# Optimization experiments

Measured on AMD Instinct MI355X. Metric: run time of the kernel, lower is better.

The kernel has to match this reference:

```python
import jax, jax.numpy as jnp
import numpy as np

B, S, H, F, E, K = 4, 2048, 512, 2048, 8, 2


def setup_inputs() -> dict:
    key = jax.random.key(0)
    ks = jax.random.split(key, 6)
    s_h = 1.0 / np.sqrt(H)
    s_f = 1.0 / np.sqrt(F)
    return {
        "x": jax.random.normal(ks[0], (B, S, H), dtype=jnp.float32),
        "router_w": jax.random.uniform(ks[1], (E, H), jnp.float32, -s_h, s_h),
        "fc1_w": jax.random.uniform(ks[2], (E, F, H), jnp.float32, -s_h, s_h),
        "fc1_b": jax.random.uniform(ks[3], (E, F), jnp.float32, -s_h, s_h),
        "fc2_w": jax.random.uniform(ks[4], (E, H, F), jnp.float32, -s_f, s_f),
        "fc2_b": jax.random.uniform(ks[5], (E, H), jnp.float32, -s_f, s_f),
    }


def reference(x, router_w, fc1_w, fc1_b, fc2_w, fc2_b):
    # Router: Linear (no bias), softmax over experts, top-k, renormalize.
    logits = jnp.einsum("bsh,eh->bse", x, router_w)           # [B,S,E]
    probs = jax.nn.softmax(logits, axis=-1)                    # [B,S,E]
    topk_p, topk_i = jax.lax.top_k(probs, K)                   # [B,S,K]
    topk_p = topk_p / (jnp.sum(topk_p, axis=-1, keepdims=True) + 1e-9)

    # Original loop runs every expert FFN on all tokens and masks;
    # mathematically identical: dense per-expert FFN, then gather+combine.
    h1 = jnp.einsum("bsh,efh->bsef", x, fc1_w) + fc1_b         # [B,S,E,F]
    a = jax.nn.gelu(h1, approximate=False)                     # exact erf GELU (torch nn.GELU default)
    y = jnp.einsum("bsef,ehf->bseh", a, fc2_w) + fc2_b         # [B,S,E,H]

    sel = jnp.take_along_axis(y, topk_i[..., None], axis=2)    # [B,S,K,H]
    output = jnp.sum(topk_p[..., None] * sel, axis=2)          # [B,S,H]
    return output, probs, topk_i
```

## Files before the change

### kernel.cpp

```cpp
#include <hip/hip_runtime.h>

#define T_TOKENS 8192
#define HD 512
#define FD 2048
#define NE 8
#define CAP 8192
#define CSTRIDE 32

#define BM 128

typedef __attribute__((ext_vector_type(8))) short short8;
typedef __attribute__((ext_vector_type(4))) float f32x4;

__device__ __forceinline__ ushort f2bf(float f) {
  union { float f; unsigned u; } v; v.f = f;
  unsigned u = v.u;
  return (ushort)((u + 0x7fffu + ((u >> 16) & 1u)) >> 16);
}

__device__ __forceinline__ unsigned pack_trunc(float lo, float hi) {
  union { float f; unsigned u; } a, b; a.f = lo; b.f = hi;
  return __builtin_amdgcn_perm(b.u, a.u, 0x07060302);
}

__global__ void cvt_bf16(const float4* __restrict__ src, ushort4* __restrict__ dst, int n4) {
  int i = blockIdx.x * blockDim.x + threadIdx.x;
  int st = gridDim.x * blockDim.x;
  for (; i < n4; i += st) {
    float4 v = src[i];
    ushort4 o;
    o.x = f2bf(v.x); o.y = f2bf(v.y); o.z = f2bf(v.z); o.w = f2bf(v.w);
    dst[i] = o;
  }
}

#define TPW 16
__global__ void router_kernel(const float* __restrict__ x, const float* __restrict__ rw,
                              float* __restrict__ probs_out, float* __restrict__ topk_out,
                              int* __restrict__ counts, int* __restrict__ bucket_tok,
                              float* __restrict__ bucket_w, int4* __restrict__ tok_info) {
  __shared__ int lcnt[NE];
  __shared__ int lbase[NE];
  __shared__ int ls_e0[64], ls_e1[64], ls_s0[64], ls_s1[64];
  __shared__ float ls_w0[64], ls_w1[64];

  int wave = threadIdx.x >> 6, lane = threadIdx.x & 63;
  if (threadIdx.x < NE) lcnt[threadIdx.x] = 0;
  __syncthreads();

  int tbase = blockIdx.x * 64;
  for (int it = 0; it < TPW; it++) {
    int lt = wave * TPW + it;
    int t = tbase + lt;
    float acc[NE];
#pragma unroll
    for (int e = 0; e < NE; e++) acc[e] = 0.f;
    const float* xr = x + (size_t)t * HD;
    for (int c = 0; c < HD; c += 64) {
      float xv = xr[c + lane];
#pragma unroll
      for (int e = 0; e < NE; e++) acc[e] += xv * rw[e * HD + c + lane];
    }
#pragma unroll
    for (int e = 0; e < NE; e++) {
#pragma unroll
      for (int s = 32; s > 0; s >>= 1) acc[e] += __shfl_xor(acc[e], s, 64);
    }
    if (lane == 0) {
      float m = acc[0];
#pragma unroll
      for (int e = 1; e < NE; e++) m = fmaxf(m, acc[e]);
      float p[NE], s = 0.f;
#pragma unroll
      for (int e = 0; e < NE; e++) { p[e] = expf(acc[e] - m); s += p[e]; }
      float inv = 1.f / s;
#pragma unroll
      for (int e = 0; e < NE; e++) { p[e] *= inv; probs_out[(size_t)t * NE + e] = p[e]; }
      int i0 = 0;
#pragma unroll
      for (int e = 1; e < NE; e++) if (p[e] > p[i0]) i0 = e;
      int i1 = (i0 == 0) ? 1 : 0;
#pragma unroll
      for (int e = 0; e < NE; e++) if (e != i0 && p[e] > p[i1]) i1 = e;
      float r = 1.f / (p[i0] + p[i1] + 1e-9f);
      topk_out[(size_t)t * 2 + 0] = (float)i0;
      topk_out[(size_t)t * 2 + 1] = (float)i1;
      ls_e0[lt] = i0; ls_e1[lt] = i1;
      ls_w0[lt] = p[i0] * r; ls_w1[lt] = p[i1] * r;
      ls_s0[lt] = atomicAdd(&lcnt[i0], 1);
      ls_s1[lt] = atomicAdd(&lcnt[i1], 1);
    }
  }
  __syncthreads();
  if (threadIdx.x < NE)
    lbase[threadIdx.x] = atomicAdd(&counts[threadIdx.x * CSTRIDE], lcnt[threadIdx.x]);
  __syncthreads();
  if (threadIdx.x < 64) {
    int lt = threadIdx.x, t = tbase + lt;
    int e0 = ls_e0[lt], e1 = ls_e1[lt];
    int g0 = lbase[e0] + ls_s0[lt];
    int g1 = lbase[e1] + ls_s1[lt];
    bucket_tok[e0 * CAP + g0] = t; bucket_w[e0 * CAP + g0] = ls_w0[lt];
    bucket_tok[e1 * CAP + g1] = t; bucket_w[e1 * CAP + g1] = ls_w1[lt];
    tok_info[t] = make_int4(e0, e1, g0, g1);
  }
}

__global__ void scan_kernel(const int* __restrict__ counts, int* __restrict__ offsets) {
  if (threadIdx.x == 0) {
    int o = 0;
#pragma unroll
    for (int e = 0; e < NE; e++) { offsets[e] = o; o += counts[e * CSTRIDE]; }
  }
}

template <int BN_, bool IS_FC1>
__global__ __launch_bounds__(256, 2)
void ffn_gemm(const ushort* __restrict__ Ab, const float* __restrict__ Bw,
              const float* __restrict__ bias, const int* __restrict__ counts,
              const int* __restrict__ offsets, const int* __restrict__ bucket_tok,
              const float* __restrict__ bucket_w, ushort* __restrict__ Aout,
              float* __restrict__ Yout, int KD, int ND) {
  constexpr int JW = BN_ / 32;
  constexpr int BCH_PT = BN_ / 32;

  int e = blockIdx.z;
  int cnt = counts[e * CSTRIDE];
  int m0 = blockIdx.y * BM;
  if (m0 >= cnt) return;
  int n0 = blockIdx.x * BN_;
  int off = offsets[e];

  __shared__ alignas(16) ushort As[8 * BM * 8];
  __shared__ alignas(16) ushort Bs[8 * BN_ * 8];

  int tid = threadIdx.x;
  int wid = tid >> 6, lid = tid & 63;
  int wm = wid >> 1, wn = wid & 1;
  int q = lid >> 4, l16 = lid & 15;

  int kc = tid & 7;
  int rbase = tid >> 3;

  const ushort* aptr[4];
  int aoff[4];
#pragma unroll
  for (int u = 0; u < 4; u++) {
    int m = rbase + u * 32;
    int mr = min(m0 + m, cnt - 1);
    int row = IS_FC1 ? bucket_tok[e * CAP + mr] : (off + mr);
    aptr[u] = Ab + (size_t)row * KD + kc * 8;
    aoff[u] = (kc * BM + (m ^ kc)) * 8;
  }
  const float* bptr[BCH_PT];
  int boff[BCH_PT];
#pragma unroll
  for (int u = 0; u < BCH_PT; u++) {
    int n = rbase + u * 32;
    bptr[u] = Bw + ((size_t)e * ND + n0 + n) * KD + kc * 8;
    boff[u] = (kc * BN_ + (n ^ kc)) * 8;
  }

  f32x4 acc[4][JW] = {};

  for (int k0 = 0; k0 < KD; k0 += 64) {
    uint4 av[4];
#pragma unroll
    for (int u = 0; u < 4; u++) av[u] = *(const uint4*)(aptr[u] + k0);
    float4 bv0[BCH_PT], bv1[BCH_PT];
#pragma unroll
    for (int u = 0; u < BCH_PT; u++) {
      bv0[u] = *(const float4*)(bptr[u] + k0);
      bv1[u] = *(const float4*)(bptr[u] + k0 + 4);
    }
#pragma unroll
    for (int u = 0; u < 4; u++) *(uint4*)&As[aoff[u]] = av[u];
#pragma unroll
    for (int u = 0; u < BCH_PT; u++) {
      uint4 o;
      o.x = pack_trunc(bv0[u].x, bv0[u].y);
      o.y = pack_trunc(bv0[u].z, bv0[u].w);
      o.z = pack_trunc(bv1[u].x, bv1[u].y);
      o.w = pack_trunc(bv1[u].z, bv1[u].w);
      *(uint4*)&Bs[boff[u]] = o;
    }
    __syncthreads();
#pragma unroll
    for (int t = 0; t < 2; t++) {
      int kcc = t * 4 + q;
      short8 af[4], bfr[JW];
#pragma unroll
      for (int i = 0; i < 4; i++) {
        int m = wm * 64 + i * 16 + l16;
        af[i] = *(const short8*)&As[((kcc * BM) + (m ^ kcc)) * 8];
      }
#pragma unroll
      for (int j = 0; j < JW; j++) {
        int n = wn * (16 * JW) + j * 16 + l16;
        bfr[j] = *(const short8*)&Bs[((kcc * BN_) + (n ^ kcc)) * 8];
      }
#pragma unroll
      for (int i = 0; i < 4; i++)
#pragma unroll
        for (int j = 0; j < JW; j++)
          acc[i][j] = __builtin_amdgcn_mfma_f32_16x16x32_bf16(af[i], bfr[j], acc[i][j], 0, 0, 0);
    }
    __syncthreads();
  }

  float bcol[JW];
#pragma unroll
  for (int j = 0; j < JW; j++)
    bcol[j] = bias[(size_t)e * ND + n0 + wn * (16 * JW) + j * 16 + l16];

  if (IS_FC1) {
    ushort* Ct = As;
#pragma unroll
    for (int i = 0; i < 4; i++) {
      __syncthreads();
#pragma unroll
      for (int j = 0; j < JW; j++)
#pragma unroll
        for (int r = 0; r < 4; r++) {
          float v = acc[i][j][r] + bcol[j];
          float g = 0.5f * v * (1.0f + erff(v * 0.70710678118654752f));
          Ct[(wm * 16 + q * 4 + r) * 136 + wn * 64 + j * 16 + l16] = f2bf(g);
        }
      __syncthreads();
#pragma unroll
      for (int u = 0; u < 2; u++) {
        int c = tid + u * 256;
        int ml = c >> 4, cc = c & 15;
        int gm = m0 + (ml >> 4) * 64 + i * 16 + (ml & 15);
        if (gm < cnt)
          *(uint4*)&Aout[(size_t)(off + gm) * ND + n0 + cc * 8] =
              *(const uint4*)&Ct[ml * 136 + cc * 8];
      }
    }
  } else {
    float* Ct = (float*)As;
#pragma unroll
    for (int i = 0; i < 4; i++) {
      __syncthreads();
#pragma unroll
      for (int r = 0; r < 4; r++) {
        int gm = m0 + wm * 64 + i * 16 + q * 4 + r;
        float wgt = bucket_w[e * CAP + min(gm, cnt - 1)];
#pragma unroll
        for (int j = 0; j < JW; j++)
          Ct[(wm * 16 + q * 4 + r) * 68 + wn * 32 + j * 16 + l16] = wgt * (acc[i][j][r] + bcol[j]);
      }
      __syncthreads();
#pragma unroll
      for (int u = 0; u < 2; u++) {
        int c = tid + u * 256;
        int ml = c >> 4, cc = c & 15;
        int gm = m0 + (ml >> 4) * 64 + i * 16 + (ml & 15);
        if (gm < cnt)
          *(float4*)&Yout[(size_t)(off + gm) * ND + n0 + cc * 4] =
              *(const float4*)&Ct[ml * 68 + cc * 4];
      }
    }
  }
}

__global__ void combine_kernel(const float4* __restrict__ Y, const int4* __restrict__ tok_info,
                               const int* __restrict__ offsets, float4* __restrict__ out) {
  int t = blockIdx.x;
  int4 ti = tok_info[t];
  int g0 = offsets[ti.x] + ti.z;
  int g1 = offsets[ti.y] + ti.w;
  int i = threadIdx.x;
  float4 a = Y[(size_t)g0 * (HD / 4) + i];
  float4 b = Y[(size_t)g1 * (HD / 4) + i];
  out[(size_t)t * (HD / 4) + i] = make_float4(a.x + b.x, a.y + b.y, a.z + b.z, a.w + b.w);
}

extern "C" void kernel_launch(void* const* d_in, const int* in_sizes, int n_in,
                              void* d_out, int out_size, void* d_ws, size_t ws_size,
                              hipStream_t stream) {
  const float* x    = (const float*)d_in[0];
  const float* rw   = (const float*)d_in[1];
  const float* fc1w = (const float*)d_in[2];
  const float* fc1b = (const float*)d_in[3];
  const float* fc2w = (const float*)d_in[4];
  const float* fc2b = (const float*)d_in[5];

  float* out   = (float*)d_out;
  float* probs = out + (size_t)T_TOKENS * HD;
  float* topk  = probs + (size_t)T_TOKENS * NE;

  char* p = (char*)d_ws;
  auto carve = [&](size_t bytes) { char* r = p; p += (bytes + 255) & ~(size_t)255; return r; };
  int*    counts     = (int*)carve(NE * CSTRIDE * sizeof(int));
  int*    offsets    = (int*)carve(NE * sizeof(int));
  int*    bucket_tok = (int*)carve((size_t)NE * CAP * sizeof(int));
  float*  bucket_w   = (float*)carve((size_t)NE * CAP * sizeof(float));
  int4*   tok_info   = (int4*)carve((size_t)T_TOKENS * sizeof(int4));
  ushort* xb   = (ushort*)carve((size_t)T_TOKENS * HD * 2);
  ushort* Abuf = (ushort*)carve((size_t)T_TOKENS * 2 * FD * 2);
  float*  Y    = (float*)carve((size_t)T_TOKENS * 2 * HD * 4);

  hipMemsetAsync(counts, 0, NE * CSTRIDE * sizeof(int), stream);
  cvt_bf16<<<2048, 256, 0, stream>>>((const float4*)x, (ushort4*)xb, T_TOKENS * HD / 4);
  router_kernel<<<T_TOKENS / 64, 256, 0, stream>>>(x, rw, probs, topk, counts, bucket_tok,
                                                   bucket_w, tok_info);
  scan_kernel<<<1, 64, 0, stream>>>(counts, offsets);
  ffn_gemm<128, true><<<dim3(FD / 128, CAP / BM, NE), 256, 0, stream>>>(
      xb, fc1w, fc1b, counts, offsets, bucket_tok, bucket_w, Abuf, nullptr, HD, FD);
  ffn_gemm<64, false><<<dim3(HD / 64, CAP / BM, NE), 256, 0, stream>>>(
      Abuf, fc2w, fc2b, counts, offsets, bucket_tok, bucket_w, nullptr, Y, FD, HD);
  combine_kernel<<<T_TOKENS, 128, 0, stream>>>((const float4*)Y, tok_info, offsets, (float4*)out);
}
```

Baseline: 351.2 us.

## Pre-convert expert weights to bf16 and stage tiles via direct global-to-LDS loads

Adds separate conversion passes that turn both expert weight tensors into bf16 once per call. The GEMM then loads A and B tiles straight into shared memory with global_load_lds instead of staging them through registers and packing floats in the loop. The LDS layout loses its XOR swizzle and becomes a plain [kchunk][row] order, which may add bank conflicts on fragment reads. The conversion passes add extra memory traffic (read 64MB fp32, write 32MB bf16) per call, and rounding now uses round-to-nearest instead of truncation.

```diff
diff --git a/kernel.cpp b/kernel.cpp
--- a/kernel.cpp
+++ b/kernel.cpp
@@ -18,9 +18,10 @@
   return (ushort)((u + 0x7fffu + ((u >> 16) & 1u)) >> 16);
 }
 
-__device__ __forceinline__ unsigned pack_trunc(float lo, float hi) {
-  union { float f; unsigned u; } a, b; a.f = lo; b.f = hi;
-  return __builtin_amdgcn_perm(b.u, a.u, 0x07060302);
+__device__ __forceinline__ void gld16(const void* g, void* l) {
+  __builtin_amdgcn_global_load_lds(
+      (const __attribute__((address_space(1))) void*)g,
+      (__attribute__((address_space(3))) void*)l, 16, 0, 0);
 }
 
 __global__ void cvt_bf16(const float4* __restrict__ src, ushort4* __restrict__ dst, int n4) {
@@ -116,13 +117,13 @@
 
 template <int BN_, bool IS_FC1>
 __global__ __launch_bounds__(256, 2)
-void ffn_gemm(const ushort* __restrict__ Ab, const float* __restrict__ Bw,
+void ffn_gemm(const ushort* __restrict__ Ab, const ushort* __restrict__ Bw,
               const float* __restrict__ bias, const int* __restrict__ counts,
               const int* __restrict__ offsets, const int* __restrict__ bucket_tok,
               const float* __restrict__ bucket_w, ushort* __restrict__ Aout,
               float* __restrict__ Yout, int KD, int ND) {
   constexpr int JW = BN_ / 32;
-  constexpr int BCH_PT = BN_ / 32;
+  constexpr int BISS = BN_ / 32;
 
   int e = blockIdx.z;
   int cnt = counts[e * CSTRIDE];
@@ -135,70 +136,51 @@
   __shared__ alignas(16) ushort Bs[8 * BN_ * 8];
 
   int tid = threadIdx.x;
-  int wid = tid >> 6, lid = tid & 63;
+  int wid = tid >> 6, lane = tid & 63;
   int wm = wid >> 1, wn = wid & 1;
-  int q = lid >> 4, l16 = lid & 15;
-
-  int kc = tid & 7;
-  int rbase = tid >> 3;
-
-  const ushort* aptr[4];
-  int aoff[4];
+  int q = lane >> 4, l16 = lane & 15;
+
+  const ushort* agp[4];
+  ushort* alp[4];
 #pragma unroll
   for (int u = 0; u < 4; u++) {
-    int m = rbase + u * 32;
+    int s = u * 4 + wid;
+    int kc = s >> 1, m = ((s & 1) << 6) + lane;
     int mr = min(m0 + m, cnt - 1);
-    int row = IS_FC1 ? bucket_tok[e * CAP + mr] : (off + mr);
-    aptr[u] = Ab + (size_t)row * KD + kc * 8;
-    aoff[u] = (kc * BM + (m ^ kc)) * 8;
-  }
-  const float* bptr[BCH_PT];
-  int boff[BCH_PT];
-#pragma unroll
-  for (int u = 0; u < BCH_PT; u++) {
-    int n = rbase + u * 32;
-    bptr[u] = Bw + ((size_t)e * ND + n0 + n) * KD + kc * 8;
-    boff[u] = (kc * BN_ + (n ^ kc)) * 8;
+    int arow = IS_FC1 ? bucket_tok[e * CAP + mr] : (off + mr);
+    agp[u] = Ab + (size_t)arow * KD + kc * 8;
+    alp[u] = As + (size_t)(s * 64 + lane) * 8;
+  }
+  const ushort* bgp[BISS];
+  ushort* blp[BISS];
+#pragma unroll
+  for (int u = 0; u < BISS; u++) {
+    int s = u * 4 + wid;
+    int kc, n;
+    if (BN_ == 128) { kc = s >> 1; n = ((s & 1) << 6) + lane; }
+    else            { kc = s;      n = lane; }
+    bgp[u] = Bw + ((size_t)e * ND + n0 + n) * KD + kc * 8;
+    blp[u] = Bs + (size_t)(s * 64 + lane) * 8;
   }
 
   f32x4 acc[4][JW] = {};
 
   for (int k0 = 0; k0 < KD; k0 += 64) {
-    uint4 av[4];
-#pragma unroll
-    for (int u = 0; u < 4; u++) av[u] = *(const uint4*)(aptr[u] + k0);
-    float4 bv0[BCH_PT], bv1[BCH_PT];
-#pragma unroll
-    for (int u = 0; u < BCH_PT; u++) {
-      bv0[u] = *(const float4*)(bptr[u] + k0);
-      bv1[u] = *(const float4*)(bptr[u] + k0 + 4);
-    }
-#pragma unroll
-    for (int u = 0; u < 4; u++) *(uint4*)&As[aoff[u]] = av[u];
-#pragma unroll
-    for (int u = 0; u < BCH_PT; u++) {
-      uint4 o;
-      o.x = pack_trunc(bv0[u].x, bv0[u].y);
-      o.y = pack_trunc(bv0[u].z, bv0[u].w);
-      o.z = pack_trunc(bv1[u].x, bv1[u].y);
-      o.w = pack_trunc(bv1[u].z, bv1[u].w);
-      *(uint4*)&Bs[boff[u]] = o;
-    }
+#pragma unroll
+    for (int u = 0; u < 4; u++) gld16(agp[u] + k0, alp[u]);
+#pragma unroll
+    for (int u = 0; u < BISS; u++) gld16(bgp[u] + k0, blp[u]);
     __syncthreads();
 #pragma unroll
     for (int t = 0; t < 2; t++) {
       int kcc = t * 4 + q;
       short8 af[4], bfr[JW];
 #pragma unroll
-      for (int i = 0; i < 4; i++) {
-        int m = wm * 64 + i * 16 + l16;
-        af[i] = *(const short8*)&As[((kcc * BM) + (m ^ kcc)) * 8];
-      }
-#pragma unroll
-      for (int j = 0; j < JW; j++) {
-        int n = wn * (16 * JW) + j * 16 + l16;
-        bfr[j] = *(const short8*)&Bs[((kcc * BN_) + (n ^ kcc)) * 8];
-      }
+      for (int i = 0; i < 4; i++)
+        af[i] = *(const short8*)&As[(kcc * BM + wm * 64 + i * 16 + l16) * 8];
+#pragma unroll
+      for (int j = 0; j < JW; j++)
+        bfr[j] = *(const short8*)&Bs[(kcc * BN_ + wn * (16 * JW) + j * 16 + l16) * 8];
 #pragma unroll
       for (int i = 0; i < 4; i++)
 #pragma unroll
@@ -298,17 +280,21 @@
   float*  bucket_w   = (float*)carve((size_t)NE * CAP * sizeof(float));
   int4*   tok_info   = (int4*)carve((size_t)T_TOKENS * sizeof(int4));
   ushort* xb   = (ushort*)carve((size_t)T_TOKENS * HD * 2);
+  ushort* w1b  = (ushort*)carve((size_t)NE * FD * HD * 2);
+  ushort* w2b  = (ushort*)carve((size_t)NE * HD * FD * 2);
   ushort* Abuf = (ushort*)carve((size_t)T_TOKENS * 2 * FD * 2);
   float*  Y    = (float*)carve((size_t)T_TOKENS * 2 * HD * 4);
 
   hipMemsetAsync(counts, 0, NE * CSTRIDE * sizeof(int), stream);
   cvt_bf16<<<2048, 256, 0, stream>>>((const float4*)x, (ushort4*)xb, T_TOKENS * HD / 4);
+  cvt_bf16<<<2048, 256, 0, stream>>>((const float4*)fc1w, (ushort4*)w1b, NE * FD * HD / 4);
+  cvt_bf16<<<2048, 256, 0, stream>>>((const float4*)fc2w, (ushort4*)w2b, NE * HD * FD / 4);
   router_kernel<<<T_TOKENS / 64, 256, 0, stream>>>(x, rw, probs, topk, counts, bucket_tok,
                                                    bucket_w, tok_info);
   scan_kernel<<<1, 64, 0, stream>>>(counts, offsets);
   ffn_gemm<128, true><<<dim3(FD / 128, CAP / BM, NE), 256, 0, stream>>>(
-      xb, fc1w, fc1b, counts, offsets, bucket_tok, bucket_w, Abuf, nullptr, HD, FD);
+      xb, w1b, fc1b, counts, offsets, bucket_tok, bucket_w, Abuf, nullptr, HD, FD);
   ffn_gemm<64, false><<<dim3(HD / 64, CAP / BM, NE), 256, 0, stream>>>(
-      Abuf, fc2w, fc2b, counts, offsets, bucket_tok, bucket_w, nullptr, Y, FD, HD);
+      Abuf, w2b, fc2b, counts, offsets, bucket_tok, bucket_w, nullptr, Y, FD, HD);
   combine_kernel<<<T_TOKENS, 128, 0, stream>>>((const float4*)Y, tok_info, offsets, (float4*)out);
 }
```

New measurement: 433.6 us. +23.5%, slower.
